# Optimization experiments

Measured on AMD Instinct MI355X. Metric: run time of the kernel, lower is better.

The kernel has to match this reference:

```python
import jax, jax.numpy as jnp
import numpy as np

HEADS = 8
EPS = 1e-5


def _layernorm(x, g, b):
    mu = jnp.mean(x, axis=-1, keepdims=True)
    var = jnp.mean(jnp.square(x - mu), axis=-1, keepdims=True)
    return (x - mu) * jax.lax.rsqrt(var + EPS) * g + b


def setup_inputs() -> dict:
    key = jax.random.key(0)
    ks = jax.random.split(key, 10)
    B, S, D = 4, 2048, 256
    d_ff = 2 * D
    s = 0.02
    return {
        "x": jax.random.normal(ks[0], (B, S, D), dtype=jnp.float32),
        "ln1_g": jnp.ones((D,), jnp.float32),
        "ln1_b": jnp.zeros((D,), jnp.float32),
        "w_qkv": jax.random.normal(ks[1], (3 * D, D), jnp.float32) * s,
        "b_qkv": jnp.zeros((3 * D,), jnp.float32),
        "w_proj": jax.random.normal(ks[2], (D, D), jnp.float32) * s,
        "b_proj": jnp.zeros((D,), jnp.float32),
        "ln2_g": jnp.ones((D,), jnp.float32),
        "ln2_b": jnp.zeros((D,), jnp.float32),
        "w1": jax.random.normal(ks[3], (d_ff, D), jnp.float32) * s,
        "b1": jnp.zeros((d_ff,), jnp.float32),
        "w2": jax.random.normal(ks[4], (D, d_ff), jnp.float32) * s,
        "b2": jnp.zeros((D,), jnp.float32),
    }


def reference(x, ln1_g, ln1_b, w_qkv, b_qkv, w_proj, b_proj,
              ln2_g, ln2_b, w1, b1, w2, b2):
    B, S, D = x.shape
    H = HEADS
    dh = D // H
    scale = dh ** -0.5

    # --- attention sublayer (pre-LN) ---
    y = _layernorm(x, ln1_g, ln1_b)
    qkv = y @ w_qkv.T + b_qkv                       # [B,S,3D]
    qkv = qkv.reshape(B, S, 3, H, dh)
    q = jnp.transpose(qkv[:, :, 0], (0, 2, 1, 3))   # [B,H,S,dh]
    k = jnp.transpose(qkv[:, :, 1], (0, 2, 1, 3))
    v = jnp.transpose(qkv[:, :, 2], (0, 2, 1, 3))
    attn = jax.nn.softmax(jnp.einsum('bhsd,bhtd->bhst', q, k) * scale, axis=-1)
    ctx = jnp.einsum('bhst,bhtd->bhsd', attn, v)    # [B,H,S,dh]
    ctx = jnp.transpose(ctx, (0, 2, 1, 3)).reshape(B, S, D)
    x = x + ctx @ w_proj.T + b_proj

    # --- FFN sublayer (pre-LN) ---
    y = _layernorm(x, ln2_g, ln2_b)
    h = jax.nn.silu(y @ w1.T + b1)                  # [B,S,2D]
    x = x + h @ w2.T + b2
    return x
```

## Files before the change

kernel.cpp:

```cpp
#include <hip/hip_runtime.h>
#include <cstddef>

constexpr int kB   = 4;
constexpr int kS   = 2048;
constexpr int kD   = 256;
constexpr int kH   = 8;
constexpr int kDH  = 32;
constexpr int kDFF = 512;
constexpr int kM   = kB * kS;
constexpr float kEps = 1e-5f;
constexpr float kScaleL2E = 0.17677669529663687f * 1.4426950408889634f;

typedef float f32x4  __attribute__((ext_vector_type(4)));
typedef short bf16x8 __attribute__((ext_vector_type(8)));
typedef unsigned short u16;
typedef unsigned int   u32;

__device__ inline u16 f2bf(float x) {
    union { float f; unsigned u; } c; c.f = x;
    const unsigned r = c.u + 0x7fffu + ((c.u >> 16) & 1u);
    return (u16)(r >> 16);
}

__device__ inline u32 pk_trunc(float lo, float hi) {
    union { float f; u32 u; } a, b; a.f = lo; b.f = hi;
    return __builtin_amdgcn_perm(b.u, a.u, 0x07060302u);
}

__global__ __launch_bounds__(256)
void ln_kernel(const float* __restrict__ x, const float* __restrict__ g,
               const float* __restrict__ b, u16* __restrict__ y)
{
    const int wave = threadIdx.x >> 6;
    const int lane = threadIdx.x & 63;
    const int row  = blockIdx.x * 4 + wave;
    const float4 v = *(const float4*)&x[(size_t)row * kD + lane * 4];
    float s1 = (v.x + v.y) + (v.z + v.w);
    float s2 = (v.x * v.x + v.y * v.y) + (v.z * v.z + v.w * v.w);
    #pragma unroll
    for (int off = 1; off < 64; off <<= 1) {
        s1 += __shfl_xor(s1, off);
        s2 += __shfl_xor(s2, off);
    }
    const float mu  = s1 * (1.0f / kD);
    const float var = s2 * (1.0f / kD) - mu * mu;
    const float inv = rsqrtf(var + kEps);
    const float4 g4 = *(const float4*)&g[lane * 4];
    const float4 b4 = *(const float4*)&b[lane * 4];
    *(ushort4*)&y[(size_t)row * kD + lane * 4] = make_ushort4(
        f2bf((v.x - mu) * inv * g4.x + b4.x),
        f2bf((v.y - mu) * inv * g4.y + b4.y),
        f2bf((v.z - mu) * inv * g4.z + b4.z),
        f2bf((v.w - mu) * inv * g4.w + b4.w));
}

template<int NT, int OUTMODE, bool RES, int KTOT>
__global__ __launch_bounds__(256)
void gemm_bf16(const u16* __restrict__ A, const float* __restrict__ Wf,
               const float* __restrict__ bias, const float* __restrict__ res,
               float* __restrict__ Cf, u16* __restrict__ Cb,
               u16* __restrict__ KbP, u16* __restrict__ VtP, int N)
{
    constexpr int BSTR = KTOT + 4;
    __shared__ u16 Bs[NT * BSTR];
    const int tid  = threadIdx.x;
    const int wave = tid >> 6;
    const int lane = tid & 63;
    const int quad = lane >> 4;
    const int l16  = lane & 15;
    const int m0 = blockIdx.x * 128;
    const int n0 = blockIdx.y * NT;

    {
        constexpr int ITS = (NT * KTOT) / 1024;
        #pragma unroll
        for (int it = 0; it < ITS; ++it) {
            const int e   = it * 1024 + tid * 4;
            const int row = e / KTOT;
            const int col = e & (KTOT - 1);
            const float4 wv = *(const float4*)&Wf[(size_t)(n0 + row) * KTOT + col];
            *(ushort4*)&Bs[row * BSTR + col] = make_ushort4(
                f2bf(wv.x), f2bf(wv.y), f2bf(wv.z), f2bf(wv.w));
        }
    }
    __syncthreads();

    f32x4 acc[2][NT / 16];
    #pragma unroll
    for (int mt = 0; mt < 2; ++mt)
        #pragma unroll
        for (int ni = 0; ni < NT / 16; ++ni) acc[mt][ni] = {0.f, 0.f, 0.f, 0.f};

    const u16* arow0 = &A[(size_t)(m0 + wave * 16 + l16) * KTOT];
    const u16* arow1 = &A[(size_t)(m0 + 64 + wave * 16 + l16) * KTOT];
    #pragma unroll 4
    for (int k0 = 0; k0 < KTOT; k0 += 32) {
        const bf16x8 a0 = *(const bf16x8*)&arow0[k0 + quad * 8];
        const bf16x8 a1 = *(const bf16x8*)&arow1[k0 + quad * 8];
        #pragma unroll
        for (int ni = 0; ni < NT / 16; ++ni) {
            const bf16x8 bf = *(const bf16x8*)&Bs[(ni * 16 + l16) * BSTR + k0 + quad * 8];
            acc[0][ni] = __builtin_amdgcn_mfma_f32_16x16x32_bf16(a0, bf, acc[0][ni], 0, 0, 0);
            acc[1][ni] = __builtin_amdgcn_mfma_f32_16x16x32_bf16(a1, bf, acc[1][ni], 0, 0, 0);
        }
    }

    #pragma unroll
    for (int mt = 0; mt < 2; ++mt) {
        #pragma unroll
        for (int ni = 0; ni < NT / 16; ++ni) {
            const float bias_v = bias[n0 + ni * 16 + l16];
            #pragma unroll
            for (int r = 0; r < 4; ++r) {
                const int m = m0 + mt * 64 + wave * 16 + quad * 4 + r;
                float v = acc[mt][ni][r] + bias_v;
                if (OUTMODE == 0) {
                    const int n = n0 + ni * 16 + l16;
                    if (RES) v += res[(size_t)m * N + n];
                    Cf[(size_t)m * N + n] = v;
                } else if (OUTMODE == 1) {
                    const int n = n0 + ni * 16 + l16;
                    v = v / (1.0f + __expf(-v));
                    Cb[(size_t)m * N + n] = f2bf(v);
                } else {
                    const int rgn = n0 >> 8;
                    const int nl  = (n0 & 255) + ni * 16 + l16;
                    const int hh  = nl >> 5, dh = nl & 31;
                    const int bb  = m >> 11, s = m & (kS - 1);
                    const int bh  = bb * kH + hh;
                    if (rgn == 0)
                        Cb[((size_t)bh * kS + s) * kDH + dh] = f2bf(v * kScaleL2E);
                    else if (rgn == 1)
                        KbP[((size_t)bh * kS + s) * kDH + dh] = f2bf(v);
                    else {
                        const int so = s & 31;
                        const int vq = (so >> 2) & 3;
                        const int vj = (so & 3) | (((so >> 4) & 1) << 2);
                        VtP[(((size_t)bh * (kS / 32) + (s >> 5)) * 4 + vq) * 256
                            + dh * 8 + vj] = f2bf(v);
                    }
                }
            }
        }
    }
}

__global__ __launch_bounds__(256)
void attn_kernel(const u16* __restrict__ Qb, const u16* __restrict__ Kb,
                 const u16* __restrict__ Vp, u16* __restrict__ ctx)
{
    __shared__ float cbuf[2][32 * 33];
    const int tid  = threadIdx.x;
    const int wave = tid >> 6;
    const int lane = tid & 63;
    const int quad = lane >> 4;
    const int l16  = lane & 15;
    const int h = blockIdx.y;
    const int b = blockIdx.z;
    const int bh = b * kH + h;
    const int qsub = wave >> 1;
    const int half = wave & 1;
    const int q0 = blockIdx.x * 64 + qsub * 32;

    bf16x8 aq[2];
    aq[0] = *(const bf16x8*)&Qb[((size_t)bh * kS + q0 + l16) * kDH + quad * 8];
    aq[1] = *(const bf16x8*)&Qb[((size_t)bh * kS + q0 + 16 + l16) * kDH + quad * 8];

    const u16* Kbase = Kb + (size_t)bh * kS * kDH;
    const u16* Vbase = Vp + (size_t)bh * (kS * 32);

    f32x4 O[2][2] = {};
    float lp[2] = {0.f, 0.f};
    const f32x4 zz = {0.f, 0.f, 0.f, 0.f};

    const int kbeg = half * (kS / 2);
    #pragma unroll 1
    for (int kt = kbeg; kt < kbeg + kS / 2; kt += 64) {
        bf16x8 kf[4];
        #pragma unroll
        for (int kg = 0; kg < 4; ++kg)
            kf[kg] = *(const bf16x8*)
                &Kbase[(size_t)(kt + kg * 16 + l16) * kDH + quad * 8];
        bf16x8 vf[2][2];
        #pragma unroll
        for (int ks = 0; ks < 2; ++ks)
            #pragma unroll
            for (int nf = 0; nf < 2; ++nf)
                vf[ks][nf] = *(const bf16x8*)
                    &Vbase[(size_t)(((kt >> 5) + ks) * 4 + quad) * 1024
                           + (nf * 16 + l16) * 8];

        #pragma unroll
        for (int qb = 0; qb < 2; ++qb) {
            f32x4 S[4];
            #pragma unroll
            for (int kg = 0; kg < 4; ++kg)
                S[kg] = __builtin_amdgcn_mfma_f32_16x16x32_bf16(kf[kg], aq[qb], zz, 0, 0, 0);

            float e0[8], e1[8];
            #pragma unroll
            for (int r = 0; r < 4; ++r) {
                e0[r]     = __builtin_amdgcn_exp2f(S[0][r]);
                e0[4 + r] = __builtin_amdgcn_exp2f(S[1][r]);
                e1[r]     = __builtin_amdgcn_exp2f(S[2][r]);
                e1[4 + r] = __builtin_amdgcn_exp2f(S[3][r]);
            }
            lp[qb] += ((e0[0] + e0[1]) + (e0[2] + e0[3]))
                    + ((e0[4] + e0[5]) + (e0[6] + e0[7]))
                    + ((e1[0] + e1[1]) + (e1[2] + e1[3]))
                    + ((e1[4] + e1[5]) + (e1[6] + e1[7]));
            union { u32 u[4]; bf16x8 v; } pA0, pA1;
            pA0.u[0] = pk_trunc(e0[0], e0[1]);
            pA0.u[1] = pk_trunc(e0[2], e0[3]);
            pA0.u[2] = pk_trunc(e0[4], e0[5]);
            pA0.u[3] = pk_trunc(e0[6], e0[7]);
            pA1.u[0] = pk_trunc(e1[0], e1[1]);
            pA1.u[1] = pk_trunc(e1[2], e1[3]);
            pA1.u[2] = pk_trunc(e1[4], e1[5]);
            pA1.u[3] = pk_trunc(e1[6], e1[7]);

            O[qb][0] = __builtin_amdgcn_mfma_f32_16x16x32_bf16(pA0.v, vf[0][0], O[qb][0], 0, 0, 0);
            O[qb][1] = __builtin_amdgcn_mfma_f32_16x16x32_bf16(pA0.v, vf[0][1], O[qb][1], 0, 0, 0);
            O[qb][0] = __builtin_amdgcn_mfma_f32_16x16x32_bf16(pA1.v, vf[1][0], O[qb][0], 0, 0, 0);
            O[qb][1] = __builtin_amdgcn_mfma_f32_16x16x32_bf16(pA1.v, vf[1][1], O[qb][1], 0, 0, 0);
        }
    }

    #pragma unroll
    for (int qb = 0; qb < 2; ++qb) {
        lp[qb] += __shfl_xor(lp[qb], 16);
        lp[qb] += __shfl_xor(lp[qb], 32);
    }

    float* cb = cbuf[qsub];
    if (half == 1) {
        #pragma unroll
        for (int qb = 0; qb < 2; ++qb)
            #pragma unroll
            for (int r = 0; r < 4; ++r) {
                const int row = qb * 16 + quad * 4 + r;
                cb[row * 33 + l16]      = O[qb][0][r];
                cb[row * 33 + 16 + l16] = O[qb][1][r];
                if (l16 == 0)
                    cb[row * 33 + 32] = __shfl(lp[qb], quad * 4 + r);
            }
    }
    __syncthreads();
    if (half == 0) {
        #pragma unroll
        for (int qb = 0; qb < 2; ++qb)
            #pragma unroll
            for (int r = 0; r < 4; ++r) {
                const int row = qb * 16 + quad * 4 + r;
                const float lq  = __shfl(lp[qb], quad * 4 + r) + cb[row * 33 + 32];
                const float inv = 1.0f / lq;
                const float o0 = O[qb][0][r] + cb[row * 33 + l16];
                const float o1 = O[qb][1][r] + cb[row * 33 + 16 + l16];
                const int q = q0 + row;
                u16* crow = ctx + ((size_t)(b * kS + q)) * kD + h * kDH;
                crow[l16]      = f2bf(o0 * inv);
                crow[16 + l16] = f2bf(o1 * inv);
            }
    }
}

extern "C" void kernel_launch(void* const* d_in, const int* in_sizes, int n_in,
                              void* d_out, int out_size, void* d_ws, size_t ws_size,
                              hipStream_t stream)
{
    const float* x      = (const float*)d_in[0];
    const float* ln1_g  = (const float*)d_in[1];
    const float* ln1_b  = (const float*)d_in[2];
    const float* w_qkv  = (const float*)d_in[3];
    const float* b_qkv  = (const float*)d_in[4];
    const float* w_proj = (const float*)d_in[5];
    const float* b_proj = (const float*)d_in[6];
    const float* ln2_g  = (const float*)d_in[7];
    const float* ln2_b  = (const float*)d_in[8];
    const float* w1     = (const float*)d_in[9];
    const float* b1     = (const float*)d_in[10];
    const float* w2     = (const float*)d_in[11];
    const float* b2     = (const float*)d_in[12];
    float* out = (float*)d_out;

    char* ws = (char*)d_ws;
    u16* Qb  = (u16*)ws;
    u16* Kb  = (u16*)(ws + ((size_t)4  << 20));
    u16* Vp  = (u16*)(ws + ((size_t)8  << 20));
    u16* ctx = (u16*)(ws + ((size_t)12 << 20));
    u16* y   = (u16*)(ws + ((size_t)16 << 20));
    u16* h   = (u16*)ws;

    const dim3 blk(256);

    ln_kernel<<<dim3(kM / 4), blk, 0, stream>>>(x, ln1_g, ln1_b, y);
    gemm_bf16<64, 2, false, 256><<<dim3(kM / 128, 12), blk, 0, stream>>>(
        y, w_qkv, b_qkv, nullptr, nullptr, Qb, Kb, Vp, 0);
    attn_kernel<<<dim3(kS / 64, kH, kB), blk, 0, stream>>>(Qb, Kb, Vp, ctx);
    gemm_bf16<32, 0, true, 256><<<dim3(kM / 128, kD / 32), blk, 0, stream>>>(
        ctx, w_proj, b_proj, x, out, nullptr, nullptr, nullptr, kD);
    ln_kernel<<<dim3(kM / 4), blk, 0, stream>>>(out, ln2_g, ln2_b, y);
    gemm_bf16<64, 1, false, 256><<<dim3(kM / 128, kDFF / 64), blk, 0, stream>>>(
        y, w1, b1, nullptr, nullptr, h, nullptr, nullptr, kDFF);
    gemm_bf16<32, 0, true, 512><<<dim3(kM / 128, kD / 32), blk, 0, stream>>>(
        h, w2, b2, out, out, nullptr, nullptr, nullptr, kD);
}
```

Baseline: 168.1 us.

## Widen attention query tile to 64 rows per wave and compute row sums via MFMA

Each wave now handles 64 query rows instead of 32, so every K/V fragment loaded from global memory is reused across four query blocks, and the grid is halved. The softmax denominator is accumulated with an extra MFMA against a ones vector instead of scalar adds plus cross-lane shuffles. The key loop also loads two 64-key tiles before computing either, which gives more loads in flight. The cost is more registers (more O accumulators and two sets of fragments), which may lower occupancy. The denominator is now summed from the bf16-truncated probabilities, the same values used in the P·V product.

After: 160.5 us. -4.5%, faster.

```diff
diff --git a/kernel.cpp b/kernel.cpp
--- a/kernel.cpp
+++ b/kernel.cpp
@@ -149,7 +149,7 @@
 void attn_kernel(const u16* __restrict__ Qb, const u16* __restrict__ Kb,
                  const u16* __restrict__ Vp, u16* __restrict__ ctx)
 {
-    __shared__ float cbuf[2][32 * 33];
+    __shared__ float cbuf[2][64 * 33];
     const int tid  = threadIdx.x;
     const int wave = tid >> 6;
     const int lane = tid & 63;
@@ -160,28 +160,28 @@
     const int bh = b * kH + h;
     const int qsub = wave >> 1;
     const int half = wave & 1;
-    const int q0 = blockIdx.x * 64 + qsub * 32;
-
-    bf16x8 aq[2];
-    aq[0] = *(const bf16x8*)&Qb[((size_t)bh * kS + q0 + l16) * kDH + quad * 8];
-    aq[1] = *(const bf16x8*)&Qb[((size_t)bh * kS + q0 + 16 + l16) * kDH + quad * 8];
+    const int q0 = blockIdx.x * 128 + qsub * 64;
+
+    bf16x8 aq[4];
+    #pragma unroll
+    for (int qb = 0; qb < 4; ++qb)
+        aq[qb] = *(const bf16x8*)
+            &Qb[((size_t)bh * kS + q0 + qb * 16 + l16) * kDH + quad * 8];
 
     const u16* Kbase = Kb + (size_t)bh * kS * kDH;
     const u16* Vbase = Vp + (size_t)bh * (kS * 32);
 
-    f32x4 O[2][2] = {};
-    float lp[2] = {0.f, 0.f};
+    f32x4 O[4][2] = {};
+    f32x4 lsum[4] = {};
     const f32x4 zz = {0.f, 0.f, 0.f, 0.f};
-
-    const int kbeg = half * (kS / 2);
-    #pragma unroll 1
-    for (int kt = kbeg; kt < kbeg + kS / 2; kt += 64) {
-        bf16x8 kf[4];
+    union { u32 u[4]; bf16x8 v; } ones;
+    ones.u[0] = ones.u[1] = ones.u[2] = ones.u[3] = 0x3F803F80u;
+
+    auto load_tile = [&](int kt, bf16x8 (&kf)[4], bf16x8 (&vf)[2][2]) {
         #pragma unroll
         for (int kg = 0; kg < 4; ++kg)
             kf[kg] = *(const bf16x8*)
                 &Kbase[(size_t)(kt + kg * 16 + l16) * kDH + quad * 8];
-        bf16x8 vf[2][2];
         #pragma unroll
         for (int ks = 0; ks < 2; ++ks)
             #pragma unroll
@@ -189,70 +189,68 @@
                 vf[ks][nf] = *(const bf16x8*)
                     &Vbase[(size_t)(((kt >> 5) + ks) * 4 + quad) * 1024
                            + (nf * 16 + l16) * 8];
-
-        #pragma unroll
-        for (int qb = 0; qb < 2; ++qb) {
-            f32x4 S[4];
-            #pragma unroll
-            for (int kg = 0; kg < 4; ++kg)
-                S[kg] = __builtin_amdgcn_mfma_f32_16x16x32_bf16(kf[kg], aq[qb], zz, 0, 0, 0);
-
-            float e0[8], e1[8];
-            #pragma unroll
-            for (int r = 0; r < 4; ++r) {
-                e0[r]     = __builtin_amdgcn_exp2f(S[0][r]);
-                e0[4 + r] = __builtin_amdgcn_exp2f(S[1][r]);
-                e1[r]     = __builtin_amdgcn_exp2f(S[2][r]);
-                e1[4 + r] = __builtin_amdgcn_exp2f(S[3][r]);
-            }
-            lp[qb] += ((e0[0] + e0[1]) + (e0[2] + e0[3]))
-                    + ((e0[4] + e0[5]) + (e0[6] + e0[7]))
-                    + ((e1[0] + e1[1]) + (e1[2] + e1[3]))
-                    + ((e1[4] + e1[5]) + (e1[6] + e1[7]));
+    };
+
+    auto comp_tile = [&](bf16x8 (&kf)[4], bf16x8 (&vf)[2][2]) {
+        #pragma unroll
+        for (int qb = 0; qb < 4; ++qb) {
+            f32x4 S0 = __builtin_amdgcn_mfma_f32_16x16x32_bf16(kf[0], aq[qb], zz, 0, 0, 0);
+            f32x4 S1 = __builtin_amdgcn_mfma_f32_16x16x32_bf16(kf[1], aq[qb], zz, 0, 0, 0);
+            f32x4 S2 = __builtin_amdgcn_mfma_f32_16x16x32_bf16(kf[2], aq[qb], zz, 0, 0, 0);
+            f32x4 S3 = __builtin_amdgcn_mfma_f32_16x16x32_bf16(kf[3], aq[qb], zz, 0, 0, 0);
+
             union { u32 u[4]; bf16x8 v; } pA0, pA1;
-            pA0.u[0] = pk_trunc(e0[0], e0[1]);
-            pA0.u[1] = pk_trunc(e0[2], e0[3]);
-            pA0.u[2] = pk_trunc(e0[4], e0[5]);
-            pA0.u[3] = pk_trunc(e0[6], e0[7]);
-            pA1.u[0] = pk_trunc(e1[0], e1[1]);
-            pA1.u[1] = pk_trunc(e1[2], e1[3]);
-            pA1.u[2] = pk_trunc(e1[4], e1[5]);
-            pA1.u[3] = pk_trunc(e1[6], e1[7]);
+            pA0.u[0] = pk_trunc(__builtin_amdgcn_exp2f(S0[0]), __builtin_amdgcn_exp2f(S0[1]));
+            pA0.u[1] = pk_trunc(__builtin_amdgcn_exp2f(S0[2]), __builtin_amdgcn_exp2f(S0[3]));
+            pA0.u[2] = pk_trunc(__builtin_amdgcn_exp2f(S1[0]), __builtin_amdgcn_exp2f(S1[1]));
+            pA0.u[3] = pk_trunc(__builtin_amdgcn_exp2f(S1[2]), __builtin_amdgcn_exp2f(S1[3]));
+            pA1.u[0] = pk_trunc(__builtin_amdgcn_exp2f(S2[0]), __builtin_amdgcn_exp2f(S2[1]));
+            pA1.u[1] = pk_trunc(__builtin_amdgcn_exp2f(S2[2]), __builtin_amdgcn_exp2f(S2[3]));
+            pA1.u[2] = pk_trunc(__builtin_amdgcn_exp2f(S3[0]), __builtin_amdgcn_exp2f(S3[1]));
+            pA1.u[3] = pk_trunc(__builtin_amdgcn_exp2f(S3[2]), __builtin_amdgcn_exp2f(S3[3]));
+
+            lsum[qb] = __builtin_amdgcn_mfma_f32_16x16x32_bf16(pA0.v, ones.v, lsum[qb], 0, 0, 0);
+            lsum[qb] = __builtin_amdgcn_mfma_f32_16x16x32_bf16(pA1.v, ones.v, lsum[qb], 0, 0, 0);
 
             O[qb][0] = __builtin_amdgcn_mfma_f32_16x16x32_bf16(pA0.v, vf[0][0], O[qb][0], 0, 0, 0);
             O[qb][1] = __builtin_amdgcn_mfma_f32_16x16x32_bf16(pA0.v, vf[0][1], O[qb][1], 0, 0, 0);
             O[qb][0] = __builtin_amdgcn_mfma_f32_16x16x32_bf16(pA1.v, vf[1][0], O[qb][0], 0, 0, 0);
             O[qb][1] = __builtin_amdgcn_mfma_f32_16x16x32_bf16(pA1.v, vf[1][1], O[qb][1], 0, 0, 0);
         }
-    }
-
-    #pragma unroll
-    for (int qb = 0; qb < 2; ++qb) {
-        lp[qb] += __shfl_xor(lp[qb], 16);
-        lp[qb] += __shfl_xor(lp[qb], 32);
+    };
+
+    const int kbeg = half * (kS / 2);
+    #pragma unroll 1
+    for (int t2 = 0; t2 < 8; ++t2) {
+        const int ktA = kbeg + t2 * 128;
+        bf16x8 kfA[4], vfA[2][2], kfB[4], vfB[2][2];
+        load_tile(ktA,      kfA, vfA);
+        load_tile(ktA + 64, kfB, vfB);
+        comp_tile(kfA, vfA);
+        comp_tile(kfB, vfB);
     }
 
     float* cb = cbuf[qsub];
     if (half == 1) {
         #pragma unroll
-        for (int qb = 0; qb < 2; ++qb)
+        for (int qb = 0; qb < 4; ++qb)
             #pragma unroll
             for (int r = 0; r < 4; ++r) {
                 const int row = qb * 16 + quad * 4 + r;
                 cb[row * 33 + l16]      = O[qb][0][r];
                 cb[row * 33 + 16 + l16] = O[qb][1][r];
                 if (l16 == 0)
-                    cb[row * 33 + 32] = __shfl(lp[qb], quad * 4 + r);
+                    cb[row * 33 + 32] = lsum[qb][r];
             }
     }
     __syncthreads();
     if (half == 0) {
         #pragma unroll
-        for (int qb = 0; qb < 2; ++qb)
+        for (int qb = 0; qb < 4; ++qb)
             #pragma unroll
             for (int r = 0; r < 4; ++r) {
                 const int row = qb * 16 + quad * 4 + r;
-                const float lq  = __shfl(lp[qb], quad * 4 + r) + cb[row * 33 + 32];
+                const float lq  = lsum[qb][r] + cb[row * 33 + 32];
                 const float inv = 1.0f / lq;
                 const float o0 = O[qb][0][r] + cb[row * 33 + l16];
                 const float o1 = O[qb][1][r] + cb[row * 33 + 16 + l16];
@@ -296,7 +294,7 @@
     ln_kernel<<<dim3(kM / 4), blk, 0, stream>>>(x, ln1_g, ln1_b, y);
     gemm_bf16<64, 2, false, 256><<<dim3(kM / 128, 12), blk, 0, stream>>>(
         y, w_qkv, b_qkv, nullptr, nullptr, Qb, Kb, Vp, 0);
-    attn_kernel<<<dim3(kS / 64, kH, kB), blk, 0, stream>>>(Qb, Kb, Vp, ctx);
+    attn_kernel<<<dim3(kS / 128, kH, kB), blk, 0, stream>>>(Qb, Kb, Vp, ctx);
     gemm_bf16<32, 0, true, 256><<<dim3(kM / 128, kD / 32), blk, 0, stream>>>(
         ctx, w_proj, b_proj, x, out, nullptr, nullptr, nullptr, kD);
     ln_kernel<<<dim3(kM / 4), blk, 0, stream>>>(out, ln2_g, ln2_b, y);
```
